# Kernel tuning notes

Hardware: AMD Instinct MI355X
Metric: run time of the kernel (lower is better)

The kernel has to match this reference:

```python
import jax, jax.numpy as jnp
import numpy as np

N, K, D = 100000, 32, 64

def setup_inputs() -> dict:
    key = jax.random.key(0)
    k1, k2, k3 = jax.random.split(key, 3)
    x = jax.random.normal(k1, (N, D), dtype=jnp.float32)
    neighbors = jax.random.randint(k2, (N, K), 0, N, dtype=jnp.int32)
    weights = jax.random.uniform(k3, (N, K), dtype=jnp.float32)
    return {"x": x, "neighbors": neighbors, "weights": weights}

def reference(x, neighbors, weights):
    # Per-node importance pooling: normalize weights over neighbors, then
    # weighted-sum gathered neighbor features. (Vectorized form of the
    # original per-node Python loop; nodes with zero total weight keep
    # unnormalized weights, matching the `if weight_sum > 0` branch.)
    wsum = weights.sum(axis=1, keepdims=True)                 # [N, 1]
    w = jnp.where(wsum > 0, weights / wsum, weights)          # [N, K]
    nbr_feats = x[neighbors]                                  # [N, K, D] gather
    pooled = jnp.einsum("nk,nkd->nd", w, nbr_feats)          # [N, D]
    return pooled
```

## Files before the change

### kernel.cpp

```cpp
#include <hip/hip_runtime.h>
#include <hip/hip_fp16.h>


#define K_NBR 32
#define D_FEAT 64

__global__ __launch_bounds__(256) void ImportancePooling_28424093564958_convert(
    const float4* __restrict__ x4, uint2* __restrict__ xh4, int n4) {
  const int i = blockIdx.x * blockDim.x + threadIdx.x;
  if (i < n4) {
    const float4 v = x4[i];
    const __half2 a = __floats2half2_rn(v.x, v.y);
    const __half2 b = __floats2half2_rn(v.z, v.w);
    uint2 u;
    u.x = *(const unsigned int*)&a;
    u.y = *(const unsigned int*)&b;
    xh4[i] = u;
  }
}

__global__ __launch_bounds__(256) void ImportancePooling_28424093564958_kernel(
    const __half2* __restrict__ xh2,
    const int* __restrict__ neighbors,
    const float* __restrict__ weights,
    float2* __restrict__ out2,
    int Nw) {
  const int wave_id = (int)((blockIdx.x * blockDim.x + threadIdx.x) >> 6);
  const int lane = threadIdx.x & 63;
  if (wave_id >= Nw) return;

  const long hbase = (long)wave_id * 64;
  const int w_bits = __float_as_int(weights[hbase + lane]);
  const int nb = neighbors[hbase + lane];

  float wsum = __int_as_float(w_bits);
  #pragma unroll
  for (int off = 16; off >= 1; off >>= 1) wsum += __shfl_xor(wsum, off, 64);
  const float inv = (wsum > 0.0f) ? (1.0f / wsum) : 1.0f;

  const int vbase = (lane & 32) << 2;
  const int sub = lane & 31;

  float accx = 0.0f, accy = 0.0f;
  #pragma unroll
  for (int k = 0; k < K_NBR; ++k) {
    const int wk_b = __builtin_amdgcn_ds_bpermute(vbase + 4 * k, w_bits);
    const int idx = __builtin_amdgcn_ds_bpermute(vbase + 4 * k, nb);
    const float wk = __int_as_float(wk_b);
    const __half2 h = xh2[(long)idx * (D_FEAT / 2) + sub];
    accx = fmaf(wk, __low2float(h), accx);
    accy = fmaf(wk, __high2float(h), accy);
  }

  float2 o;
  o.x = accx * inv;
  o.y = accy * inv;
  out2[hbase + lane] = o;
}

__global__ __launch_bounds__(256) void ImportancePooling_28424093564958_f32(
    const float* __restrict__ x, const int* __restrict__ neighbors,
    const float* __restrict__ weights, float* __restrict__ out, int N) {
  const int wave_id = (int)((blockIdx.x * blockDim.x + threadIdx.x) >> 6);
  const int lane = threadIdx.x & 63;
  if (wave_id >= N) return;
  const long hbase = (long)wave_id * K_NBR;
  int packed;
  if (lane < K_NBR) {
    packed = __float_as_int(weights[hbase + lane]);
  } else {
    packed = neighbors[hbase + (lane - K_NBR)];
  }
  float acc = 0.0f, wsum = 0.0f;
  #pragma unroll
  for (int k = 0; k < K_NBR; ++k) {
    const float wk = __int_as_float(__builtin_amdgcn_readlane(packed, k));
    const int idx = __builtin_amdgcn_readlane(packed, K_NBR + k);
    wsum += wk;
    acc += wk * x[(long)idx * D_FEAT + lane];
  }
  const float inv = (wsum > 0.0f) ? (1.0f / wsum) : 1.0f;
  out[(long)wave_id * D_FEAT + lane] = acc * inv;
}

extern "C" void kernel_launch(void* const* d_in, const int* in_sizes, int n_in,
                              void* d_out, int out_size, void* d_ws, size_t ws_size,
                              hipStream_t stream) {
  const float* x = (const float*)d_in[0];
  const int* neighbors = (const int*)d_in[1];
  const float* weights = (const float*)d_in[2];

  const int N = in_sizes[0] / D_FEAT;
  const size_t xh_bytes = (size_t)N * D_FEAT * sizeof(__half);

  if (ws_size >= xh_bytes && (N % 2) == 0) {
    const int n4 = N * D_FEAT / 4;
    ImportancePooling_28424093564958_convert<<<(n4 + 255) / 256, 256, 0, stream>>>(
        (const float4*)x, (uint2*)d_ws, n4);

    const int Nw = N / 2;
    const int block = 256;
    const int grid = (Nw * 64 + block - 1) / block;
    ImportancePooling_28424093564958_kernel<<<grid, block, 0, stream>>>(
        (const __half2*)d_ws, neighbors, weights, (float2*)d_out, Nw);
  } else {
    const int block = 256;
    const int grid = (N * 64 + block - 1) / block;
    ImportancePooling_28424093564958_f32<<<grid, block, 0, stream>>>(
        x, neighbors, weights, (float*)d_out, N);
  }
}
```

Baseline: 136.1 us.

## Process eight nodes per wave with 16-byte fp16 gathers per lane

The main kernel now maps eight nodes to each wave, with 8 lanes per node, instead of two nodes per wave. Each lane gathers a 16-byte chunk (8 half values) of a neighbor row per step and keeps eight accumulators. Weights and neighbor indices are loaded in a transposed pattern and redistributed with ds_bpermute. The aim is fewer, wider gather transactions and less per-node shuffle overhead. Nontemporal loads and stores and a launch-bounds occupancy hint are also added; the tradeoffs are more registers per thread and a stricter N%8 condition for the fast path.

```diff
diff --git a/kernel.cpp b/kernel.cpp
--- a/kernel.cpp
+++ b/kernel.cpp
@@ -5,57 +5,107 @@
 #define K_NBR 32
 #define D_FEAT 64
 
+typedef float f32x4 __attribute__((ext_vector_type(4)));
+typedef unsigned int u32x2 __attribute__((ext_vector_type(2)));
+typedef unsigned int u32x4 __attribute__((ext_vector_type(4)));
+
+static __device__ __forceinline__ __half2 u32_as_h2(unsigned int u) {
+  __half2 h;
+  __builtin_memcpy(&h, &u, 4);
+  return h;
+}
+
+static __device__ __forceinline__ unsigned int h2_as_u32(__half2 h) {
+  unsigned int u;
+  __builtin_memcpy(&u, &h, 4);
+  return u;
+}
+
 __global__ __launch_bounds__(256) void ImportancePooling_28424093564958_convert(
-    const float4* __restrict__ x4, uint2* __restrict__ xh4, int n4) {
+    const f32x4* __restrict__ x4, u32x2* __restrict__ xh4, int n4) {
   const int i = blockIdx.x * blockDim.x + threadIdx.x;
   if (i < n4) {
-    const float4 v = x4[i];
+    const f32x4 v = __builtin_nontemporal_load(&x4[i]);
     const __half2 a = __floats2half2_rn(v.x, v.y);
     const __half2 b = __floats2half2_rn(v.z, v.w);
-    uint2 u;
-    u.x = *(const unsigned int*)&a;
-    u.y = *(const unsigned int*)&b;
+    u32x2 u;
+    u.x = h2_as_u32(a);
+    u.y = h2_as_u32(b);
     xh4[i] = u;
   }
 }
 
-__global__ __launch_bounds__(256) void ImportancePooling_28424093564958_kernel(
-    const __half2* __restrict__ xh2,
+__global__ __launch_bounds__(256, 8) void ImportancePooling_28424093564958_kernel(
+    const u32x4* __restrict__ xh4,
     const int* __restrict__ neighbors,
     const float* __restrict__ weights,
-    float2* __restrict__ out2,
+    f32x4* __restrict__ out4,
     int Nw) {
   const int wave_id = (int)((blockIdx.x * blockDim.x + threadIdx.x) >> 6);
   const int lane = threadIdx.x & 63;
   if (wave_id >= Nw) return;
 
-  const long hbase = (long)wave_id * 64;
-  const int w_bits = __float_as_int(weights[hbase + lane]);
-  const int nb = neighbors[hbase + lane];
+  const int g = lane >> 3;
+  const int f = lane & 7;
+  const int gb4 = g << 2;
+  const long hbase = (long)wave_id * 256;
 
-  float wsum = __int_as_float(w_bits);
-  #pragma unroll
-  for (int off = 16; off >= 1; off >>= 1) wsum += __shfl_xor(wsum, off, 64);
-  const float inv = (wsum > 0.0f) ? (1.0f / wsum) : 1.0f;
-
-  const int vbase = (lane & 32) << 2;
-  const int sub = lane & 31;
-
-  float accx = 0.0f, accy = 0.0f;
-  #pragma unroll
-  for (int k = 0; k < K_NBR; ++k) {
-    const int wk_b = __builtin_amdgcn_ds_bpermute(vbase + 4 * k, w_bits);
-    const int idx = __builtin_amdgcn_ds_bpermute(vbase + 4 * k, nb);
-    const float wk = __int_as_float(wk_b);
-    const __half2 h = xh2[(long)idx * (D_FEAT / 2) + sub];
-    accx = fmaf(wk, __low2float(h), accx);
-    accy = fmaf(wk, __high2float(h), accy);
+  int wb[4], nb[4];
+  {
+    const long e0 = hbase + f * 32 + g;
+    wb[0] = __float_as_int(__builtin_nontemporal_load(&weights[e0]));
+    wb[1] = __float_as_int(__builtin_nontemporal_load(&weights[e0 + 8]));
+    wb[2] = __float_as_int(__builtin_nontemporal_load(&weights[e0 + 16]));
+    wb[3] = __float_as_int(__builtin_nontemporal_load(&weights[e0 + 24]));
+    nb[0] = __builtin_nontemporal_load(&neighbors[e0]);
+    nb[1] = __builtin_nontemporal_load(&neighbors[e0 + 8]);
+    nb[2] = __builtin_nontemporal_load(&neighbors[e0 + 16]);
+    nb[3] = __builtin_nontemporal_load(&neighbors[e0 + 24]);
   }
 
-  float2 o;
-  o.x = accx * inv;
-  o.y = accy * inv;
-  out2[hbase + lane] = o;
+  float s = __int_as_float(wb[0]) + __int_as_float(wb[1]) +
+            __int_as_float(wb[2]) + __int_as_float(wb[3]);
+  s += __shfl_xor(s, 8, 64);
+  s += __shfl_xor(s, 16, 64);
+  s += __shfl_xor(s, 32, 64);
+  const float invp = (s > 0.0f) ? (1.0f / s) : 1.0f;
+  const float inv = __int_as_float(
+      __builtin_amdgcn_ds_bpermute(gb4, __float_as_int(invp)));
+
+  float acc[8];
+#pragma unroll
+  for (int i = 0; i < 8; ++i) acc[i] = 0.0f;
+
+#pragma unroll
+  for (int k = 0; k < K_NBR; ++k) {
+    const int addr = ((k & 7) << 5) + gb4;
+    const float wk =
+        __int_as_float(__builtin_amdgcn_ds_bpermute(addr, wb[k >> 3]));
+    const int idx = __builtin_amdgcn_ds_bpermute(addr, nb[k >> 3]);
+    const u32x4 h = xh4[(unsigned)idx * 8u + (unsigned)f];
+    const __half2 p0 = u32_as_h2(h.x);
+    const __half2 p1 = u32_as_h2(h.y);
+    const __half2 p2 = u32_as_h2(h.z);
+    const __half2 p3 = u32_as_h2(h.w);
+    acc[0] = fmaf(wk, __low2float(p0), acc[0]);
+    acc[1] = fmaf(wk, __high2float(p0), acc[1]);
+    acc[2] = fmaf(wk, __low2float(p1), acc[2]);
+    acc[3] = fmaf(wk, __high2float(p1), acc[3]);
+    acc[4] = fmaf(wk, __low2float(p2), acc[4]);
+    acc[5] = fmaf(wk, __high2float(p2), acc[5]);
+    acc[6] = fmaf(wk, __low2float(p3), acc[6]);
+    acc[7] = fmaf(wk, __high2float(p3), acc[7]);
+  }
+
+  f32x4 o0, o1;
+  o0.x = acc[0] * inv; o0.y = acc[1] * inv;
+  o0.z = acc[2] * inv; o0.w = acc[3] * inv;
+  o1.x = acc[4] * inv; o1.y = acc[5] * inv;
+  o1.z = acc[6] * inv; o1.w = acc[7] * inv;
+  const unsigned obase =
+      ((unsigned)wave_id * 8u + (unsigned)g) * 16u + (unsigned)f * 2u;
+  __builtin_nontemporal_store(o0, &out4[obase]);
+  __builtin_nontemporal_store(o1, &out4[obase + 1]);
 }
 
 __global__ __launch_bounds__(256) void ImportancePooling_28424093564958_f32(
@@ -72,7 +122,7 @@
     packed = neighbors[hbase + (lane - K_NBR)];
   }
   float acc = 0.0f, wsum = 0.0f;
-  #pragma unroll
+#pragma unroll
   for (int k = 0; k < K_NBR; ++k) {
     const float wk = __int_as_float(__builtin_amdgcn_readlane(packed, k));
     const int idx = __builtin_amdgcn_readlane(packed, K_NBR + k);
@@ -93,16 +143,16 @@
   const int N = in_sizes[0] / D_FEAT;
   const size_t xh_bytes = (size_t)N * D_FEAT * sizeof(__half);
 
-  if (ws_size >= xh_bytes && (N % 2) == 0) {
+  if (ws_size >= xh_bytes && (N % 8) == 0) {
     const int n4 = N * D_FEAT / 4;
     ImportancePooling_28424093564958_convert<<<(n4 + 255) / 256, 256, 0, stream>>>(
-        (const float4*)x, (uint2*)d_ws, n4);
+        (const f32x4*)x, (u32x2*)d_ws, n4);
 
-    const int Nw = N / 2;
+    const int Nw = N / 8;
     const int block = 256;
     const int grid = (Nw * 64 + block - 1) / block;
     ImportancePooling_28424093564958_kernel<<<grid, block, 0, stream>>>(
-        (const __half2*)d_ws, neighbors, weights, (float2*)d_out, Nw);
+        (const u32x4*)d_ws, neighbors, weights, (f32x4*)d_out, Nw);
   } else {
     const int block = 256;
     const int grid = (N * 64 + block - 1) / block;
```

After: 150.7 us. +10.7%, slower.
